# Kernel tuning notes

Hardware: AMD Instinct MI355X
Metric: run time of the kernel (lower is better)

The kernel has to match this reference:

```python
import jax, jax.numpy as jnp
import numpy as np

# Nemotron-H Mamba2 mixer decoder layer (prefill path, zero initial states,
# full context lengths). Dims per init_kwargs.
B, S, H = 1, 256, 4096
NH, P, G, N, K = 128, 64, 8, 128, 4   # num_heads, head_dim, n_groups, ssm_state_size, conv_kernel
D_INNER = NH * P                      # 8192
D_STATE = G * N                       # 1024
CONV_DIM = D_INNER + 2 * D_STATE      # 10240
IN_OUT = D_INNER + CONV_DIM + NH      # 18560
EPS = 1e-6


def setup_inputs() -> dict:
    key = jax.random.key(0)
    ks = jax.random.split(key, 8)
    sc = 0.02
    return {
        "hidden_states": jax.random.normal(ks[0], (B, S, H), jnp.float32),
        "conv_state": jnp.zeros((B, CONV_DIM, K - 1), jnp.float32),
        "ssm_state": jnp.zeros((B, NH, P, N), jnp.float32),
        "norm_weight": jnp.ones((H,), jnp.float32),
        "w_in": jax.random.normal(ks[1], (IN_OUT, H), jnp.float32) * sc,
        "conv_w": jax.random.normal(ks[2], (CONV_DIM, K), jnp.float32) * 0.2,
        "conv_b": jnp.zeros((CONV_DIM,), jnp.float32),
        "A_log": jax.random.uniform(ks[3], (NH,), jnp.float32, 0.0, 1.0),
        "D_param": jax.random.normal(ks[4], (NH,), jnp.float32) * 0.1,
        "dt_bias": jax.random.normal(ks[5], (NH,), jnp.float32) * 0.1,
        "ssm_norm_weight": jnp.ones((D_INNER,), jnp.float32),
        "w_out": jax.random.normal(ks[6], (H, D_INNER), jnp.float32) * sc,
    }


def _rmsnorm(x, w, eps=EPS):
    var = jnp.mean(x * x, axis=-1, keepdims=True)
    return x * jax.lax.rsqrt(var + eps) * w


def reference(hidden_states, conv_state, ssm_state, norm_weight, w_in, conv_w,
              conv_b, A_log, D_param, dt_bias, ssm_norm_weight, w_out):
    resid = hidden_states
    h = _rmsnorm(hidden_states, norm_weight)           # pre-mixer RMSNorm
    proj = jnp.einsum('bsh,oh->bso', h, w_in)          # in_proj [B,S,18560]
    gate = proj[..., :D_INNER]
    xconv = proj[..., D_INNER:D_INNER + CONV_DIM]
    dt = proj[..., D_INNER + CONV_DIM:]                # [B,S,NH]

    # depthwise causal conv1d, initial left context = conv_state
    xc = jnp.swapaxes(xconv, 1, 2)                     # [B,CONV_DIM,S]
    xpad = jnp.concatenate([conv_state, xc], axis=-1)  # [B,CONV_DIM,S+K-1]
    conv_state_out = xpad[:, :, -(K - 1):]
    y = conv_b[None, :, None]
    for j in range(K):                                 # K=4 taps, unrolled
        y = y + conv_w[:, j][None, :, None] * xpad[:, :, j:j + S]
    y = jax.nn.silu(jnp.swapaxes(y, 1, 2))             # [B,S,CONV_DIM]

    xs = y[..., :D_INNER].reshape(B, S, NH, P)
    Bs = y[..., D_INNER:D_INNER + D_STATE].reshape(B, S, G, N)
    Cs = y[..., D_INNER + D_STATE:].reshape(B, S, G, N)

    A = -jnp.exp(A_log)                                # [NH]
    dtp = jax.nn.softplus(dt + dt_bias)                # [B,S,NH]
    rep = NH // G
    Bh = jnp.repeat(Bs, rep, axis=2)                   # [B,S,NH,N]
    Ch = jnp.repeat(Cs, rep, axis=2)

    def step(state, inp):
        x_t, b_t, c_t, dt_t = inp                      # [B,NH,P],[B,NH,N],[B,NH,N],[B,NH]
        dA = jnp.exp(dt_t * A)                         # [B,NH]
        state = state * dA[..., None, None] + (dt_t[..., None] * x_t)[..., None] * b_t[:, :, None, :]
        y_t = jnp.einsum('bhpn,bhn->bhp', state, c_t)
        return state, y_t

    inps = (jnp.swapaxes(xs, 0, 1), jnp.swapaxes(Bh, 0, 1),
            jnp.swapaxes(Ch, 0, 1), jnp.swapaxes(dtp, 0, 1))
    ssm_state_out, ys = jax.lax.scan(step, ssm_state, inps)
    ys = jnp.swapaxes(ys, 0, 1) + D_param[None, None, :, None] * xs
    ssm_out = ys.reshape(B, S, D_INNER)

    # gated grouped RMSNorm (group_size = D_INNER // G = 1024)
    gated = ssm_out * jax.nn.silu(gate)
    gsize = D_INNER // G
    gg = gated.reshape(B, S, D_INNER // gsize, gsize)
    var = jnp.mean(gg * gg, axis=-1, keepdims=True)
    normed = (gg * jax.lax.rsqrt(var + EPS)).reshape(B, S, D_INNER) * ssm_norm_weight

    out = jnp.einsum('bsd,hd->bsh', normed, w_out)     # out_proj
    return resid + out, conv_state_out, ssm_state_out
```

## Files before the change

kernel.cpp:

```cpp
#include <hip/hip_runtime.h>
#include <hip/hip_bf16.h>

#define Sq 256
#define Hd 4096
#define NH 128
#define Pd 64
#define Gg 8
#define Nn 128
#define D_INNER 8192
#define D_STATE 1024
#define CONV_DIM 10240
#define IN_OUT 18560
#define DT_COL0 18432
#define EPSI 1e-6f

typedef _Float16 f16x8 __attribute__((ext_vector_type(8)));
typedef _Float16 f16x2 __attribute__((ext_vector_type(2)));
typedef float f32x4 __attribute__((ext_vector_type(4)));

__device__ inline ushort f2h(float f) {
  _Float16 h = (_Float16)f;
  return __builtin_bit_cast(ushort, h);
}
__device__ inline float h2f(ushort u) {
  return (float)__builtin_bit_cast(_Float16, u);
}
__device__ inline ushort f2h_lo(float f, ushort hi) {
  float hf = (float)__builtin_bit_cast(_Float16, hi);
  _Float16 l = (_Float16)(f - hf);
  return __builtin_bit_cast(ushort, l);
}
__device__ inline f16x2 pkrtz(float a, float b) {
  return __builtin_bit_cast(f16x2, __builtin_amdgcn_cvt_pkrtz(a, b));
}

__global__ __launch_bounds__(256) void rmsnorm_k(const float* __restrict__ x,
                                                 const float* __restrict__ w,
                                                 ushort* __restrict__ h_hi,
                                                 ushort* __restrict__ h_lo) {
  int s = blockIdx.x, t = threadIdx.x;
  const float4* row = reinterpret_cast<const float4*>(x + (size_t)s * Hd);
  const float4* wv  = reinterpret_cast<const float4*>(w);
  float4 v[4];
  float ss = 0.f;
#pragma unroll
  for (int i = 0; i < 4; i++) {
    v[i] = row[t + i * 256];
    ss += v[i].x * v[i].x + v[i].y * v[i].y + v[i].z * v[i].z + v[i].w * v[i].w;
  }
#pragma unroll
  for (int off = 32; off > 0; off >>= 1) ss += __shfl_xor(ss, off);
  __shared__ float red[4];
  if ((t & 63) == 0) red[t >> 6] = ss;
  __syncthreads();
  ss = red[0] + red[1] + red[2] + red[3];
  float scale = rsqrtf(ss * (1.f / (float)Hd) + EPSI);
  ushort4* hh = reinterpret_cast<ushort4*>(h_hi + (size_t)s * Hd);
  ushort4* hl = reinterpret_cast<ushort4*>(h_lo + (size_t)s * Hd);
#pragma unroll
  for (int i = 0; i < 4; i++) {
    float4 wi = wv[t + i * 256];
    float f0 = v[i].x * scale * wi.x, f1 = v[i].y * scale * wi.y;
    float f2 = v[i].z * scale * wi.z, f3 = v[i].w * scale * wi.w;
    ushort4 oh, ol;
    oh.x = f2h(f0); ol.x = f2h_lo(f0, oh.x);
    oh.y = f2h(f1); ol.y = f2h_lo(f1, oh.y);
    oh.z = f2h(f2); ol.z = f2h_lo(f2, oh.z);
    oh.w = f2h(f3); ol.w = f2h_lo(f3, oh.w);
    hh[t + i * 256] = oh;
    hl[t + i * 256] = ol;
  }
}

__global__ __launch_bounds__(256) void gemm_t128(const ushort* __restrict__ A,
                                                 const float* __restrict__ B,
                                                 float* __restrict__ C0,
                                                 ushort* __restrict__ Cp,
                                                 int ldc, int K, int kLen) {
  __shared__ __align__(16) ushort As[2][128 * 32];
  __shared__ __align__(16) ushort Bs[2][128 * 32];
  int t = threadIdx.x;
  int wave = t >> 6, lane = t & 63;
  int wr = wave >> 1, wc = wave & 1;
  int frow = lane & 15, gq = lane >> 4;
  int coltile = blockIdx.x >> 1;
  int rowBase = (blockIdx.x & 1) * 128;
  int bcol = coltile * 128;
  int z = blockIdx.z;
  int kStart = z * kLen;

  int ar = t >> 2;
  int ax = (ar >> 1) & 3;
  const ushort* ApG0 = A + (size_t)(rowBase + ar) * K + kStart + ((t & 3) ^ ax) * 8;
  const ushort* ApG1 = ApG0 + (size_t)64 * K;
  char* dstA0 = (char*)&As[0][0] + wave * 1024;
  char* dstA1 = (char*)&As[0][0] + 4096 + wave * 1024;

  int brow = t >> 1, bhalf = t & 1;
  int bx = (brow >> 1) & 3;
  const float* BpG = B + (size_t)(bcol + brow) * K + kStart + bhalf * 16;
  int bslot0 = ((2 * bhalf) ^ bx) * 16;
  int bslot1 = ((2 * bhalf + 1) ^ bx) * 16;
  float4 rb[4];

  f32x4 acc[4][4] = {};
  const int NT = kLen / 32;

#define ISSUE_B(kk) { _Pragma("unroll") for (int j = 0; j < 4; ++j) \
                        rb[j] = *(const float4*)(BpG + (kk) + j * 4); }
#define DMA_A(p, kk) { \
    __builtin_amdgcn_global_load_lds( \
        (const __attribute__((address_space(1))) void*)(ApG0 + (kk)), \
        (__attribute__((address_space(3))) void*)(dstA0 + (p) * 8192), 16, 0, 0); \
    __builtin_amdgcn_global_load_lds( \
        (const __attribute__((address_space(1))) void*)(ApG1 + (kk)), \
        (__attribute__((address_space(3))) void*)(dstA1 + (p) * 8192), 16, 0, 0); }
#define WRITE_B(p) { \
    union { f16x2 h2[8]; uint4 q[2]; } u; \
    u.h2[0] = pkrtz(rb[0].x, rb[0].y); u.h2[1] = pkrtz(rb[0].z, rb[0].w); \
    u.h2[2] = pkrtz(rb[1].x, rb[1].y); u.h2[3] = pkrtz(rb[1].z, rb[1].w); \
    u.h2[4] = pkrtz(rb[2].x, rb[2].y); u.h2[5] = pkrtz(rb[2].z, rb[2].w); \
    u.h2[6] = pkrtz(rb[3].x, rb[3].y); u.h2[7] = pkrtz(rb[3].z, rb[3].w); \
    char* bb = (char*)&Bs[0][0] + (p) * 8192 + brow * 64; \
    *(uint4*)(bb + bslot0) = u.q[0]; \
    *(uint4*)(bb + bslot1) = u.q[1]; }

  ISSUE_B(0)
  DMA_A(0, 0)
  WRITE_B(0)
  __syncthreads();

  for (int i = 0; i < NT; ++i) {
    int cur = i & 1;
    if (i + 1 < NT) {
      ISSUE_B((i + 1) * 32)
      DMA_A(cur ^ 1, (i + 1) * 32)
    }
    f16x8 af[4], bf[4];
#pragma unroll
    for (int m = 0; m < 4; ++m) {
      int row = wr * 64 + m * 16 + frow;
      af[m] = *(const f16x8*)((const char*)&As[0][0] + cur * 8192 + row * 64 +
                              ((gq ^ ((row >> 1) & 3)) * 16));
    }
#pragma unroll
    for (int n = 0; n < 4; ++n) {
      int row = wc * 64 + n * 16 + frow;
      bf[n] = *(const f16x8*)((const char*)&Bs[0][0] + cur * 8192 + row * 64 +
                              ((gq ^ ((row >> 1) & 3)) * 16));
    }
#pragma unroll
    for (int m = 0; m < 4; ++m)
#pragma unroll
      for (int n = 0; n < 4; ++n)
        acc[m][n] = __builtin_amdgcn_mfma_f32_16x16x32_f16(af[m], bf[n], acc[m][n], 0, 0, 0);
    __builtin_amdgcn_sched_barrier(0);
    if (i + 1 < NT) WRITE_B(cur ^ 1)
    __syncthreads();
  }
#undef ISSUE_B
#undef DMA_A
#undef WRITE_B

  if (z == 0) {
#pragma unroll
    for (int m = 0; m < 4; ++m) {
      int row0 = rowBase + wr * 64 + m * 16 + (lane >> 4) * 4;
#pragma unroll
      for (int n = 0; n < 4; ++n) {
        int col = bcol + wc * 64 + n * 16 + frow;
#pragma unroll
        for (int r = 0; r < 4; ++r)
          C0[(size_t)(row0 + r) * ldc + col] = acc[m][n][r];
      }
    }
  } else {
    ushort* Cz = Cp + (size_t)(z - 1) * Sq * ldc;
#pragma unroll
    for (int m = 0; m < 4; ++m) {
      int row0 = rowBase + wr * 64 + m * 16 + (lane >> 4) * 4;
#pragma unroll
      for (int n = 0; n < 4; ++n) {
        int col = bcol + wc * 64 + n * 16 + frow;
#pragma unroll
        for (int r = 0; r < 4; ++r)
          Cz[(size_t)(row0 + r) * ldc + col] = f2h(acc[m][n][r]);
      }
    }
  }
}

template<int BN, bool SPLIT>
__global__ __launch_bounds__(256) void gemm_mfma(const ushort* __restrict__ A_hi,
                                                 const ushort* __restrict__ A_lo,
                                                 const float* __restrict__ B,
                                                 float* __restrict__ C,
                                                 int ldc, int K, int kLen,
                                                 int bcol0, int M) {
  constexpr int BK = 64;
  constexpr int LDA = 72;
  constexpr int N_REP = BN / 32;
  constexpr int BQN = (BN == 128) ? 8 : 4;
  __shared__ __align__(16) ushort As[64 * LDA];
  __shared__ __align__(16) ushort Bs[BN * LDA];
  __shared__ __align__(16) ushort AsL[SPLIT ? 64 * LDA : 1];
  __shared__ __align__(16) ushort BsL[SPLIT ? BN * LDA : 1];

  int t = threadIdx.x;
  int wave = t >> 6, lane = t & 63;
  int wr = wave >> 1, wc = wave & 1;
  int frow = lane & 15, fk = (lane >> 4) * 8;
  int rowBase = blockIdx.x * 64;
  int bcol = bcol0 + blockIdx.y * BN;
  int ccol = blockIdx.y * BN;
  int kStart = blockIdx.z * kLen;
  C += (size_t)blockIdx.z * M * ldc;

  int arow = t >> 2, ak = (t & 3) * 16;
  const ushort* Ap  = A_hi + (size_t)(rowBase + arow) * K + ak;
  const ushort* ApL = SPLIT ? (A_lo + (size_t)(rowBase + arow) * K + ak) : nullptr;

  int brow, bq;
  if constexpr (BN == 128) { brow = t >> 1; bq = (t & 1) * 32; }
  else                     { brow = t >> 2; bq = (t & 3) * 16; }
  const float* Bp = B + (size_t)(bcol + brow) * K + bq;

  f32x4 acc[2][N_REP] = {};
  uint4 aPre[2], aPreL[2];
  float4 bPre[BQN];

  auto loadK = [&](int kk) {
    aPre[0] = *reinterpret_cast<const uint4*>(Ap + kk);
    aPre[1] = *reinterpret_cast<const uint4*>(Ap + kk + 8);
    if constexpr (SPLIT) {
      aPreL[0] = *reinterpret_cast<const uint4*>(ApL + kk);
      aPreL[1] = *reinterpret_cast<const uint4*>(ApL + kk + 8);
    }
#pragma unroll
    for (int j = 0; j < BQN; ++j)
      bPre[j] = *reinterpret_cast<const float4*>(Bp + kk + j * 4);
  };

  loadK(kStart);
  for (int ki = 0; ki < kLen; ki += BK) {
    __syncthreads();
    *reinterpret_cast<uint4*>(&As[arow * LDA + ak])     = aPre[0];
    *reinterpret_cast<uint4*>(&As[arow * LDA + ak + 8]) = aPre[1];
    if constexpr (SPLIT) {
      *reinterpret_cast<uint4*>(&AsL[arow * LDA + ak])     = aPreL[0];
      *reinterpret_cast<uint4*>(&AsL[arow * LDA + ak + 8]) = aPreL[1];
    }
    {
      ushort hb[BQN * 4];
      ushort lb[SPLIT ? BQN * 4 : 1];
      const float* bf = reinterpret_cast<const float*>(bPre);
#pragma unroll
      for (int j = 0; j < BQN * 4; ++j) {
        hb[j] = f2h(bf[j]);
        if constexpr (SPLIT) lb[j] = f2h_lo(bf[j], hb[j]);
      }
#pragma unroll
      for (int j = 0; j < BQN / 2; ++j)
        *reinterpret_cast<uint4*>(&Bs[brow * LDA + bq + j * 8]) =
            reinterpret_cast<const uint4*>(hb)[j];
      if constexpr (SPLIT) {
#pragma unroll
        for (int j = 0; j < BQN / 2; ++j)
          *reinterpret_cast<uint4*>(&BsL[brow * LDA + bq + j * 8]) =
              reinterpret_cast<const uint4*>(lb)[j];
      }
    }
    __syncthreads();
    if (ki + BK < kLen) loadK(kStart + ki + BK);
    f16x8 af[2][2], bfv[N_REP][2];
    f16x8 afL[SPLIT ? 2 : 1][2], bfL[SPLIT ? N_REP : 1][2];
#pragma unroll
    for (int m = 0; m < 2; ++m)
#pragma unroll
      for (int kh = 0; kh < 2; ++kh) {
        af[m][kh] = *reinterpret_cast<const f16x8*>(
            &As[(wr * 32 + m * 16 + frow) * LDA + kh * 32 + fk]);
        if constexpr (SPLIT)
          afL[m][kh] = *reinterpret_cast<const f16x8*>(
              &AsL[(wr * 32 + m * 16 + frow) * LDA + kh * 32 + fk]);
      }
#pragma unroll
    for (int n = 0; n < N_REP; ++n)
#pragma unroll
      for (int kh = 0; kh < 2; ++kh) {
        bfv[n][kh] = *reinterpret_cast<const f16x8*>(
            &Bs[(wc * (BN / 2) + n * 16 + frow) * LDA + kh * 32 + fk]);
        if constexpr (SPLIT)
          bfL[n][kh] = *reinterpret_cast<const f16x8*>(
              &BsL[(wc * (BN / 2) + n * 16 + frow) * LDA + kh * 32 + fk]);
      }
#pragma unroll
    for (int kh = 0; kh < 2; ++kh)
#pragma unroll
      for (int m = 0; m < 2; ++m)
#pragma unroll
        for (int n = 0; n < N_REP; ++n) {
          acc[m][n] = __builtin_amdgcn_mfma_f32_16x16x32_f16(af[m][kh], bfv[n][kh], acc[m][n], 0, 0, 0);
          if constexpr (SPLIT) {
            acc[m][n] = __builtin_amdgcn_mfma_f32_16x16x32_f16(af[m][kh], bfL[n][kh], acc[m][n], 0, 0, 0);
            acc[m][n] = __builtin_amdgcn_mfma_f32_16x16x32_f16(afL[m][kh], bfv[n][kh], acc[m][n], 0, 0, 0);
          }
        }
  }

#pragma unroll
  for (int m = 0; m < 2; ++m) {
    int row0 = rowBase + wr * 32 + m * 16 + (lane >> 4) * 4;
#pragma unroll
    for (int n = 0; n < N_REP; ++n) {
      int col = ccol + wc * (BN / 2) + n * 16 + frow;
#pragma unroll
      for (int r = 0; r < 4; ++r)
        C[(size_t)(row0 + r) * ldc + col] = acc[m][n][r];
    }
  }
}

__global__ __launch_bounds__(256) void reduce_in_k(float* __restrict__ proj,
                                                   const ushort* __restrict__ pp) {
  int i = blockIdx.x * 256 + threadIdx.x;
  const size_t PL = (size_t)Sq * IN_OUT;
  float4 o = reinterpret_cast<const float4*>(proj)[i];
#pragma unroll
  for (int zz = 0; zz < 3; ++zz) {
    ushort4 hv = reinterpret_cast<const ushort4*>(pp + zz * PL)[i];
    o.x += h2f(hv.x); o.y += h2f(hv.y); o.z += h2f(hv.z); o.w += h2f(hv.w);
  }
  reinterpret_cast<float4*>(proj)[i] = o;
}

__global__ __launch_bounds__(256) void conv_silu_k(const float* __restrict__ proj,
                                                   const float* __restrict__ cstate,
                                                   const float* __restrict__ cw,
                                                   const float* __restrict__ cb,
                                                   float* __restrict__ y) {
  int c = blockIdx.x * 256 + threadIdx.x;
  int s = blockIdx.y;
  float acc = cb[c];
  float4 w4 = *reinterpret_cast<const float4*>(cw + c * 4);
  float wj[4] = {w4.x, w4.y, w4.z, w4.w};
#pragma unroll
  for (int j = 0; j < 4; j++) {
    int si = s + j - 3;
    float v = (si < 0) ? cstate[c * 3 + (si + 3)]
                       : proj[(size_t)si * IN_OUT + D_INNER + c];
    acc += wj[j] * v;
  }
  float sig = 1.f / (1.f + expf(-acc));
  y[(size_t)s * CONV_DIM + c] = acc * sig;
}

__global__ __launch_bounds__(256) void conv_state_out_k(const float* __restrict__ proj,
                                                        float* __restrict__ out1) {
  int idx = blockIdx.x * 256 + threadIdx.x;
  int c = idx / 3, tt = idx % 3;
  out1[idx] = proj[(size_t)(Sq - 3 + tt) * IN_OUT + D_INNER + c];
}

__global__ __launch_bounds__(256) void dt_k(const float* __restrict__ dtfix,
                                            const float* __restrict__ dt_bias,
                                            float* __restrict__ dtp) {
  int idx = blockIdx.x * 256 + threadIdx.x;
  int hh = idx & 127;
  float v = dt_bias[hh];
#pragma unroll
  for (int zz = 0; zz < 32; ++zz) v += dtfix[zz * 32768 + idx];
  dtp[idx] = (v > 20.f) ? v : log1pf(expf(v));
}

#define CS 16
__global__ __launch_bounds__(256) void ssm_scan_k(const float* __restrict__ y_conv,
                                                  const float* __restrict__ dtp,
                                                  const float* __restrict__ sstate_in,
                                                  const float* __restrict__ A_log,
                                                  const float* __restrict__ D_param,
                                                  float* __restrict__ ys_out,
                                                  float* __restrict__ sstate_out) {
  int h = blockIdx.x >> 1;
  int pb = (blockIdx.x & 1) * 32;
  int t = threadIdx.x;
  int ng = t & 7, pl = t >> 3;
  int g = h >> 4;
  float A = -expf(A_log[h]);
  float Dp = D_param[h];

  float st[16];
  {
    const float* sp = sstate_in + ((size_t)h * Pd + pb + pl) * Nn + ng * 16;
#pragma unroll
    for (int i = 0; i < 16; i += 4) {
      float4 v = *reinterpret_cast<const float4*>(sp + i);
      st[i] = v.x; st[i + 1] = v.y; st[i + 2] = v.z; st[i + 3] = v.w;
    }
  }

  __shared__ float ybuf[CS][296];
  __shared__ float dts[CS];
  int lr = t >> 4;
  int lc = t & 15;

  for (int ch = 0; ch < Sq / CS; ++ch) {
    int s0 = ch * CS;
    __syncthreads();
    const float* rowp = y_conv + (size_t)(s0 + lr) * CONV_DIM;
#pragma unroll
    for (int j = 0; j < 5; ++j) {
      int c = lc + 16 * j;
      if (c < 72) {
        const float* src;
        if (c < 8)       src = rowp + h * 64 + pb + c * 4;
        else if (c < 40) src = rowp + D_INNER + g * 128 + (c - 8) * 4;
        else             src = rowp + D_INNER + D_STATE + g * 128 + (c - 40) * 4;
        *reinterpret_cast<float4*>(&ybuf[lr][c * 4]) = *reinterpret_cast<const float4*>(src);
      }
    }
    if (t < CS) dts[t] = dtp[(s0 + t) * NH + h];
    __syncthreads();

#pragma unroll 4
    for (int stp = 0; stp < CS; ++stp) {
      float dt = dts[stp];
      float dA = expf(dt * A);
      float x0 = ybuf[stp][pl];
      float dtx = dt * x0;
      float y0 = 0.f;
#pragma unroll
      for (int i = 0; i < 16; ++i) {
        float b = ybuf[stp][32 + ng * 16 + i];
        float c = ybuf[stp][160 + ng * 16 + i];
        st[i] = st[i] * dA + dtx * b;
        y0 += st[i] * c;
      }
      y0 += __shfl_xor(y0, 1); y0 += __shfl_xor(y0, 2); y0 += __shfl_xor(y0, 4);
      if (ng == 0)
        ys_out[(size_t)(s0 + stp) * D_INNER + h * 64 + pb + pl] = y0 + Dp * x0;
    }
  }

  float* so = sstate_out + ((size_t)h * Pd + pb + pl) * Nn + ng * 16;
#pragma unroll
  for (int i = 0; i < 16; i += 4)
    *reinterpret_cast<float4*>(so + i) = make_float4(st[i], st[i + 1], st[i + 2], st[i + 3]);
}

__global__ __launch_bounds__(256) void gated_norm_k(const float* __restrict__ ys,
                                                    const float* __restrict__ proj,
                                                    const float* __restrict__ w,
                                                    ushort* __restrict__ out_h) {
  int s = blockIdx.x, g = blockIdx.y, t = threadIdx.x;
  float vals[4];
  float ss = 0.f;
#pragma unroll
  for (int i = 0; i < 4; i++) {
    int d = g * 1024 + i * 256 + t;
    float gate = proj[(size_t)s * IN_OUT + d];
    float v = ys[(size_t)s * D_INNER + d] * (gate / (1.f + expf(-gate)));
    vals[i] = v;
    ss += v * v;
  }
#pragma unroll
  for (int off = 32; off > 0; off >>= 1) ss += __shfl_xor(ss, off);
  __shared__ float red[4];
  if ((t & 63) == 0) red[t >> 6] = ss;
  __syncthreads();
  ss = red[0] + red[1] + red[2] + red[3];
  float scale = rsqrtf(ss * (1.f / 1024.f) + EPSI);
#pragma unroll
  for (int i = 0; i < 4; i++) {
    int d = g * 1024 + i * 256 + t;
    out_h[(size_t)s * D_INNER + d] = f2h(vals[i] * scale * w[d]);
  }
}

__global__ __launch_bounds__(256) void reduce_out_k(const float* __restrict__ p0,
                                                    const ushort* __restrict__ pph,
                                                    const float* __restrict__ hidden,
                                                    float* __restrict__ out0) {
  int i = blockIdx.x * 256 + threadIdx.x;
  const size_t PL = (size_t)Sq * Hd;
  float4 o = reinterpret_cast<const float4*>(hidden)[i];
  float4 a = reinterpret_cast<const float4*>(p0)[i];
  o.x += a.x; o.y += a.y; o.z += a.z; o.w += a.w;
#pragma unroll
  for (int zz = 0; zz < 15; ++zz) {
    ushort4 hv = reinterpret_cast<const ushort4*>(pph + zz * PL)[i];
    o.x += h2f(hv.x); o.y += h2f(hv.y); o.z += h2f(hv.z); o.w += h2f(hv.w);
  }
  reinterpret_cast<float4*>(out0)[i] = o;
}

extern "C" void kernel_launch(void* const* d_in, const int* in_sizes, int n_in,
                              void* d_out, int out_size, void* d_ws, size_t ws_size,
                              hipStream_t stream) {
  const float* hidden    = (const float*)d_in[0];
  const float* cstate_in = (const float*)d_in[1];
  const float* sstate_in = (const float*)d_in[2];
  const float* norm_w    = (const float*)d_in[3];
  const float* w_in      = (const float*)d_in[4];
  const float* conv_w    = (const float*)d_in[5];
  const float* conv_b    = (const float*)d_in[6];
  const float* A_log     = (const float*)d_in[7];
  const float* D_param   = (const float*)d_in[8];
  const float* dt_bias   = (const float*)d_in[9];
  const float* ssm_nw    = (const float*)d_in[10];
  const float* w_out     = (const float*)d_in[11];

  float* out0 = (float*)d_out;
  float* out1 = out0 + (size_t)Sq * Hd;
  float* out2 = out1 + (size_t)CONV_DIM * 3;

  ushort* h_hi  = (ushort*)d_ws;
  ushort* h_lo  = h_hi + (size_t)Sq * Hd;
  float*  proj  = (float*)(h_lo + (size_t)Sq * Hd);
  ushort* pp_in = (ushort*)(proj + (size_t)Sq * IN_OUT);
  float*  y_conv = (float*)pp_in;
  float*  dtp   = y_conv + (size_t)Sq * CONV_DIM;
  float*  ys    = dtp + (size_t)Sq * NH;
  ushort* ys_h  = (ushort*)(ys + (size_t)Sq * D_INNER);
  float*  dtfix = (float*)(ys_h + (size_t)Sq * D_INNER);
  float*  op0    = (float*)d_ws;
  ushort* pp_out = (ushort*)(op0 + (size_t)Sq * Hd);

  rmsnorm_k<<<Sq, 256, 0, stream>>>(hidden, norm_w, h_hi, h_lo);
  gemm_t128<<<dim3(2 * (IN_OUT / 128), 1, 4), 256, 0, stream>>>(
      h_hi, w_in, proj, pp_in, IN_OUT, Hd, Hd / 4);
  reduce_in_k<<<(Sq * IN_OUT / 4) / 256, 256, 0, stream>>>(proj, pp_in);
  gemm_mfma<64, true><<<dim3(4, 2, 32), 256, 0, stream>>>(
      h_hi, h_lo, w_in, dtfix, NH, Hd, Hd / 32, DT_COL0, Sq);
  conv_silu_k<<<dim3(CONV_DIM / 256, Sq), 256, 0, stream>>>(proj, cstate_in, conv_w, conv_b, y_conv);
  conv_state_out_k<<<(CONV_DIM * 3) / 256, 256, 0, stream>>>(proj, out1);
  dt_k<<<(Sq * NH) / 256, 256, 0, stream>>>(dtfix, dt_bias, dtp);
  ssm_scan_k<<<NH * 2, 256, 0, stream>>>(y_conv, dtp, sstate_in, A_log, D_param, ys, out2);
  gated_norm_k<<<dim3(Sq, Gg), 256, 0, stream>>>(ys, proj, ssm_nw, ys_h);
  gemm_t128<<<dim3(2 * (Hd / 128), 1, 16), 256, 0, stream>>>(
      ys_h, w_out, op0, pp_out, Hd, D_INNER, D_INNER / 16);
  reduce_out_k<<<(Sq * Hd / 4) / 256, 256, 0, stream>>>(op0, pp_out, hidden, out0);
}
```

Before: 350.7 us.

## Fuse conv-state and dt kernels into neighbors; split SSM scan across 4 blocks per head

Folds the conv_state output copy into an extra grid row of the conv kernel, and moves the dt split-K reduction plus softplus into the SSM scan kernel, removing two launches. The scan now uses 4 blocks per head with 16 state-lanes of 8 elements each, so 512 blocks run instead of 256, with vectorized LDS reads of B/C. This raises parallelism on the serial scan at the cost of redundant B/C loads per block and a recomputed dt reduction in every block of a head.

```diff
diff --git a/kernel.cpp b/kernel.cpp
--- a/kernel.cpp
+++ b/kernel.cpp
@@ -338,9 +338,17 @@
                                                    const float* __restrict__ cstate,
                                                    const float* __restrict__ cw,
                                                    const float* __restrict__ cb,
-                                                   float* __restrict__ y) {
+                                                   float* __restrict__ y,
+                                                   float* __restrict__ out1) {
+  int s = blockIdx.y;
+  if (s == Sq) {
+    int c = blockIdx.x * 256 + threadIdx.x;
+#pragma unroll
+    for (int tt = 0; tt < 3; ++tt)
+      out1[c * 3 + tt] = proj[(size_t)(Sq - 3 + tt) * IN_OUT + D_INNER + c];
+    return;
+  }
   int c = blockIdx.x * 256 + threadIdx.x;
-  int s = blockIdx.y;
   float acc = cb[c];
   float4 w4 = *reinterpret_cast<const float4*>(cw + c * 4);
   float wj[4] = {w4.x, w4.y, w4.z, w4.w};
@@ -355,51 +363,34 @@
   y[(size_t)s * CONV_DIM + c] = acc * sig;
 }
 
-__global__ __launch_bounds__(256) void conv_state_out_k(const float* __restrict__ proj,
-                                                        float* __restrict__ out1) {
-  int idx = blockIdx.x * 256 + threadIdx.x;
-  int c = idx / 3, tt = idx % 3;
-  out1[idx] = proj[(size_t)(Sq - 3 + tt) * IN_OUT + D_INNER + c];
-}
-
-__global__ __launch_bounds__(256) void dt_k(const float* __restrict__ dtfix,
-                                            const float* __restrict__ dt_bias,
-                                            float* __restrict__ dtp) {
-  int idx = blockIdx.x * 256 + threadIdx.x;
-  int hh = idx & 127;
-  float v = dt_bias[hh];
-#pragma unroll
-  for (int zz = 0; zz < 32; ++zz) v += dtfix[zz * 32768 + idx];
-  dtp[idx] = (v > 20.f) ? v : log1pf(expf(v));
-}
-
 #define CS 16
 __global__ __launch_bounds__(256) void ssm_scan_k(const float* __restrict__ y_conv,
-                                                  const float* __restrict__ dtp,
+                                                  const float* __restrict__ dtfix,
+                                                  const float* __restrict__ dt_bias,
                                                   const float* __restrict__ sstate_in,
                                                   const float* __restrict__ A_log,
                                                   const float* __restrict__ D_param,
                                                   float* __restrict__ ys_out,
                                                   float* __restrict__ sstate_out) {
-  int h = blockIdx.x >> 1;
-  int pb = (blockIdx.x & 1) * 32;
+  int h = blockIdx.x >> 2;
+  int pb = (blockIdx.x & 3) * 16;
   int t = threadIdx.x;
-  int ng = t & 7, pl = t >> 3;
+  int ng = t & 15, pl = t >> 4;
   int g = h >> 4;
   float A = -expf(A_log[h]);
   float Dp = D_param[h];
-
-  float st[16];
+  float bias = dt_bias[h];
+
+  float st[8];
   {
-    const float* sp = sstate_in + ((size_t)h * Pd + pb + pl) * Nn + ng * 16;
-#pragma unroll
-    for (int i = 0; i < 16; i += 4) {
-      float4 v = *reinterpret_cast<const float4*>(sp + i);
-      st[i] = v.x; st[i + 1] = v.y; st[i + 2] = v.z; st[i + 3] = v.w;
-    }
-  }
-
-  __shared__ float ybuf[CS][296];
+    const float* sp = sstate_in + ((size_t)h * Pd + pb + pl) * Nn + ng * 8;
+    float4 v = *reinterpret_cast<const float4*>(sp);
+    float4 w = *reinterpret_cast<const float4*>(sp + 4);
+    st[0] = v.x; st[1] = v.y; st[2] = v.z; st[3] = v.w;
+    st[4] = w.x; st[5] = w.y; st[6] = w.z; st[7] = w.w;
+  }
+
+  __shared__ __align__(16) float ybuf[CS][272];
   __shared__ float dts[CS];
   int lr = t >> 4;
   int lc = t & 15;
@@ -411,15 +402,23 @@
 #pragma unroll
     for (int j = 0; j < 5; ++j) {
       int c = lc + 16 * j;
-      if (c < 72) {
+      if (c < 68) {
         const float* src;
-        if (c < 8)       src = rowp + h * 64 + pb + c * 4;
-        else if (c < 40) src = rowp + D_INNER + g * 128 + (c - 8) * 4;
-        else             src = rowp + D_INNER + D_STATE + g * 128 + (c - 40) * 4;
-        *reinterpret_cast<float4*>(&ybuf[lr][c * 4]) = *reinterpret_cast<const float4*>(src);
-      }
-    }
-    if (t < CS) dts[t] = dtp[(s0 + t) * NH + h];
+        int off;
+        if (c < 4)       { src = rowp + h * 64 + pb;                      off = c * 4; }
+        else if (c < 36) { src = rowp + D_INNER + g * 128;                off = (c - 4) * 4; }
+        else             { src = rowp + D_INNER + D_STATE + g * 128;      off = (c - 36) * 4; }
+        int dst = (c < 4) ? c * 4 : (c < 36 ? 16 + (c - 4) * 4 : 144 + (c - 36) * 4);
+        *reinterpret_cast<float4*>(&ybuf[lr][dst]) = *reinterpret_cast<const float4*>(src + off);
+      }
+    }
+    if (t < CS) {
+      float v = bias;
+      int idx = (s0 + t) * NH + h;
+#pragma unroll
+      for (int zz = 0; zz < 32; ++zz) v += dtfix[zz * (Sq * NH) + idx];
+      dts[t] = (v > 20.f) ? v : log1pf(expf(v));
+    }
     __syncthreads();
 
 #pragma unroll 4
@@ -428,24 +427,29 @@
       float dA = expf(dt * A);
       float x0 = ybuf[stp][pl];
       float dtx = dt * x0;
-      float y0 = 0.f;
-#pragma unroll
-      for (int i = 0; i < 16; ++i) {
-        float b = ybuf[stp][32 + ng * 16 + i];
-        float c = ybuf[stp][160 + ng * 16 + i];
-        st[i] = st[i] * dA + dtx * b;
-        y0 += st[i] * c;
-      }
-      y0 += __shfl_xor(y0, 1); y0 += __shfl_xor(y0, 2); y0 += __shfl_xor(y0, 4);
+      float4 b0 = *reinterpret_cast<const float4*>(&ybuf[stp][16 + ng * 8]);
+      float4 b1 = *reinterpret_cast<const float4*>(&ybuf[stp][16 + ng * 8 + 4]);
+      float4 c0 = *reinterpret_cast<const float4*>(&ybuf[stp][144 + ng * 8]);
+      float4 c1 = *reinterpret_cast<const float4*>(&ybuf[stp][144 + ng * 8 + 4]);
+      float y0;
+      st[0] = st[0] * dA + dtx * b0.x;  y0  = st[0] * c0.x;
+      st[1] = st[1] * dA + dtx * b0.y;  y0 += st[1] * c0.y;
+      st[2] = st[2] * dA + dtx * b0.z;  y0 += st[2] * c0.z;
+      st[3] = st[3] * dA + dtx * b0.w;  y0 += st[3] * c0.w;
+      st[4] = st[4] * dA + dtx * b1.x;  y0 += st[4] * c1.x;
+      st[5] = st[5] * dA + dtx * b1.y;  y0 += st[5] * c1.y;
+      st[6] = st[6] * dA + dtx * b1.z;  y0 += st[6] * c1.z;
+      st[7] = st[7] * dA + dtx * b1.w;  y0 += st[7] * c1.w;
+      y0 += __shfl_xor(y0, 1); y0 += __shfl_xor(y0, 2);
+      y0 += __shfl_xor(y0, 4); y0 += __shfl_xor(y0, 8);
       if (ng == 0)
         ys_out[(size_t)(s0 + stp) * D_INNER + h * 64 + pb + pl] = y0 + Dp * x0;
     }
   }
 
-  float* so = sstate_out + ((size_t)h * Pd + pb + pl) * Nn + ng * 16;
-#pragma unroll
-  for (int i = 0; i < 16; i += 4)
-    *reinterpret_cast<float4*>(so + i) = make_float4(st[i], st[i + 1], st[i + 2], st[i + 3]);
+  float* so = sstate_out + ((size_t)h * Pd + pb + pl) * Nn + ng * 8;
+  *reinterpret_cast<float4*>(so)     = make_float4(st[0], st[1], st[2], st[3]);
+  *reinterpret_cast<float4*>(so + 4) = make_float4(st[4], st[5], st[6], st[7]);
 }
 
 __global__ __launch_bounds__(256) void gated_norm_k(const float* __restrict__ ys,
@@ -532,10 +536,10 @@
   reduce_in_k<<<(Sq * IN_OUT / 4) / 256, 256, 0, stream>>>(proj, pp_in);
   gemm_mfma<64, true><<<dim3(4, 2, 32), 256, 0, stream>>>(
       h_hi, h_lo, w_in, dtfix, NH, Hd, Hd / 32, DT_COL0, Sq);
-  conv_silu_k<<<dim3(CONV_DIM / 256, Sq), 256, 0, stream>>>(proj, cstate_in, conv_w, conv_b, y_conv);
-  conv_state_out_k<<<(CONV_DIM * 3) / 256, 256, 0, stream>>>(proj, out1);
-  dt_k<<<(Sq * NH) / 256, 256, 0, stream>>>(dtfix, dt_bias, dtp);
-  ssm_scan_k<<<NH * 2, 256, 0, stream>>>(y_conv, dtp, sstate_in, A_log, D_param, ys, out2);
+  conv_silu_k<<<dim3(CONV_DIM / 256, Sq + 1), 256, 0, stream>>>(
+      proj, cstate_in, conv_w, conv_b, y_conv, out1);
+  ssm_scan_k<<<NH * 4, 256, 0, stream>>>(y_conv, dtfix, dt_bias, sstate_in,
+                                         A_log, D_param, ys, out2);
   gated_norm_k<<<dim3(Sq, Gg), 256, 0, stream>>>(ys, proj, ssm_nw, ys_h);
   gemm_t128<<<dim3(2 * (Hd / 128), 1, 16), 256, 0, stream>>>(
       ys_h, w_out, op0, pp_out, Hd, D_INNER, D_INNER / 16);
```

Measured after the change: 349.0 us. No clear change (-0.5%).
